# Kernel optimization log

Measured on AMD Instinct MI355X. Metric: run time of the kernel, lower is better.

## Reference

```python
import math
import jax, jax.numpy as jnp
import numpy as np

N, H, E, K = 8192, 2048, 8, 2
CF = 1.25


def setup_inputs() -> dict:
    key = jax.random.key(0)
    ks = jax.random.split(key, 5)
    s1 = 1.0 / math.sqrt(H)
    s2 = 1.0 / math.sqrt(2 * H)
    return {
        "tokens": jax.random.normal(ks[0], (N, H), jnp.float32),
        "Wr": jax.random.normal(ks[1], (E, H), jnp.float32) * s1,   # router: logits = x @ Wr.T + br
        "br": jnp.zeros((E,), jnp.float32),
        "W1": jax.random.normal(ks[2], (E, H, 2 * H), jnp.float32) * s1,
        "b1": jnp.zeros((E, 2 * H), jnp.float32),
        "W2": jax.random.normal(ks[3], (E, 2 * H, H), jnp.float32) * s2,
        "b2": jnp.zeros((E, H), jnp.float32),
    }


def reference(tokens, Wr, br, W1, b1, W2, b2):
    n = tokens.shape[0]
    cap = max(1, math.ceil(CF * n / E))  # per-expert capacity (static)

    # --- router + top-k ---
    logits = tokens @ Wr.T + br                         # [N, E]
    scores, expert_ids = jax.lax.top_k(logits, K)       # [N, K]
    probs = jax.nn.softmax(scores, axis=-1)

    # --- flatten dispatches and sort by expert (stable, like the torch code) ---
    flat_e = expert_ids.reshape(-1)                     # [N*K]
    flat_t = jnp.repeat(jnp.arange(n), K)               # [N*K]
    flat_s = probs.reshape(-1).astype(tokens.dtype)     # [N*K]
    order = jnp.argsort(flat_e)                         # jnp.argsort is stable
    se, st, ss = flat_e[order], flat_t[order], flat_s[order]

    # --- capacity-limited gather: fixed [E, cap] index grid ---
    seg_start = jnp.searchsorted(se, jnp.arange(E))     # [E] first slot of each expert segment
    counts = jnp.bincount(se, length=E)                 # [E] tokens routed to each expert
    slot = jnp.arange(cap)
    idx = jnp.clip(seg_start[:, None] + slot[None, :], 0, n * K - 1)  # [E, cap]
    valid = slot[None, :] < jnp.minimum(counts, cap)[:, None]          # [E, cap]
    tok_idx = st[idx]                                   # [E, cap] source token ids
    w = jnp.where(valid, ss[idx], 0.0)[..., None]       # [E, cap, 1] combine weights (0 => dropped)

    # --- grouped per-expert FFN (GEMM over [E, cap, H]) ---
    x = tokens[tok_idx]                                 # [E, cap, H]
    h = jax.nn.gelu(jnp.einsum('ech,ehf->ecf', x, W1) + b1[:, None, :], approximate=False)
    y = jnp.einsum('ecf,efh->ech', h, W2) + b2[:, None, :]

    # --- weighted scatter-add combine ---
    out = jnp.zeros_like(tokens).at[tok_idx.reshape(-1)].add((y * w).reshape(-1, tokens.shape[-1]))
    return out
```

## Files before the change

### kernel.cpp

```cpp
#include <hip/hip_runtime.h>
#include <hip/hip_bf16.h>
#include <math.h>

#define NTOK 8192
#define HDIM 2048
#define NEXP 8
#define TOPK 2
#define CAP  1280
#define FF   4096

typedef float  f32x4  __attribute__((ext_vector_type(4)));
typedef __bf16 bf16x8 __attribute__((ext_vector_type(8)));

__device__ __forceinline__ ushort f2bf(float f) {
    union { float f; unsigned u; } c; c.f = f;
    unsigned u = c.u;
    unsigned r = (u + 0x7FFFu + ((u >> 16) & 1u)) >> 16;
    return (ushort)r;
}
__device__ __forceinline__ float bf2f(ushort h) {
    union { unsigned u; float f; } c; c.u = ((unsigned)h) << 16;
    return c.f;
}

__global__ void k_convert(const float* __restrict__ src, ushort* __restrict__ dst) {
    int i = (blockIdx.x * 256 + threadIdx.x) * 8;
    float4 a = *(const float4*)(src + i);
    float4 b = *(const float4*)(src + i + 4);
    uint4 o;
    o.x = (unsigned)f2bf(a.x) | ((unsigned)f2bf(a.y) << 16);
    o.y = (unsigned)f2bf(a.z) | ((unsigned)f2bf(a.w) << 16);
    o.z = (unsigned)f2bf(b.x) | ((unsigned)f2bf(b.y) << 16);
    o.w = (unsigned)f2bf(b.z) | ((unsigned)f2bf(b.w) << 16);
    *(uint4*)(dst + i) = o;
}

__global__ void k_router(const float* __restrict__ tokens, const float* __restrict__ Wr,
                         const float* __restrict__ br, int* __restrict__ eids,
                         float* __restrict__ probs) {
    int wave = threadIdx.x >> 6, lane = threadIdx.x & 63;
    int t = blockIdx.x * 4 + wave;
    const float* tp = tokens + (size_t)t * HDIM;
    double acc[NEXP];
    #pragma unroll
    for (int e = 0; e < NEXP; ++e) acc[e] = 0.0;
    for (int j = 0; j < HDIM / 64; ++j) {
        float x = tp[j * 64 + lane];
        #pragma unroll
        for (int e = 0; e < NEXP; ++e)
            acc[e] += (double)x * (double)Wr[e * HDIM + j * 64 + lane];
    }
    #pragma unroll
    for (int e = 0; e < NEXP; ++e) {
        #pragma unroll
        for (int off = 32; off; off >>= 1) acc[e] += __shfl_xor(acc[e], off, 64);
    }
    if (lane == 0) {
        float lg[NEXP];
        #pragma unroll
        for (int e = 0; e < NEXP; ++e) lg[e] = (float)acc[e] + br[e];
        int e0 = 0; float s0 = lg[0];
        #pragma unroll
        for (int e = 1; e < NEXP; ++e) if (lg[e] > s0) { s0 = lg[e]; e0 = e; }
        int e1 = -1; float s1 = -1e30f;
        #pragma unroll
        for (int e = 0; e < NEXP; ++e) if (e != e0 && lg[e] > s1) { s1 = lg[e]; e1 = e; }
        float ex = expf(s1 - s0);
        float den = 1.f + ex;
        eids[t * 2] = e0; eids[t * 2 + 1] = e1;
        probs[t * 2] = 1.f / den; probs[t * 2 + 1] = ex / den;
    }
}

__global__ void k_assign(const int* __restrict__ eids, int* __restrict__ tok_map,
                         int* __restrict__ dest) {
    __shared__ int cnt[64][NEXP];
    int l = threadIdx.x;
    for (int i = l; i < NEXP * CAP; i += 64) tok_map[i] = 0;
    int c[NEXP];
    #pragma unroll
    for (int e = 0; e < NEXP; ++e) c[e] = 0;
    const int base = l * 256;
    for (int i = 0; i < 256; ++i) {
        int ee = eids[base + i];
        #pragma unroll
        for (int e = 0; e < NEXP; ++e) c[e] += (ee == e);
    }
    #pragma unroll
    for (int e = 0; e < NEXP; ++e) cnt[l][e] = c[e];
    __syncthreads();
    if (l < NEXP) {
        int run = 0;
        for (int b = 0; b < 64; ++b) { int v = cnt[b][l]; cnt[b][l] = run; run += v; }
    }
    __syncthreads();
    int off[NEXP];
    #pragma unroll
    for (int e = 0; e < NEXP; ++e) off[e] = cnt[l][e];
    for (int i = 0; i < 256; ++i) {
        int d = base + i;
        int ee = eids[d];
        int r = -1;
        #pragma unroll
        for (int e = 0; e < NEXP; ++e) { bool m = (ee == e); if (m) r = off[e]; off[e] += m; }
        if (r < CAP) { tok_map[ee * CAP + r] = d >> 1; dest[d] = ee * CAP + r; }
        else dest[d] = -1;
    }
}

__global__ void k_transpose(const float* __restrict__ src, ushort* __restrict__ dst,
                            int Kd, int Nd) {
    __shared__ float t[32][33];
    int e = blockIdx.z;
    int k0 = blockIdx.x * 32, n0 = blockIdx.y * 32;
    const float* s = src + (size_t)e * Kd * Nd;
    ushort* d = dst + (size_t)e * Kd * Nd;
    int tid = threadIdx.x;
    #pragma unroll
    for (int i = 0; i < 4; ++i) {
        int idx = i * 256 + tid; int kk = idx >> 5, nn = idx & 31;
        t[kk][nn] = s[(size_t)(k0 + kk) * Nd + n0 + nn];
    }
    __syncthreads();
    #pragma unroll
    for (int i = 0; i < 4; ++i) {
        int idx = i * 256 + tid; int nn = idx >> 5, kk = idx & 31;
        d[(size_t)(n0 + nn) * Kd + k0 + kk] = f2bf(t[kk][nn]);
    }
}

#define LDA 40
template<bool DOGELU, bool GATHER>
__global__ __launch_bounds__(256) void k_gemm(const ushort* __restrict__ A,
                                              const int* __restrict__ tmap,
                                              const ushort* __restrict__ B,
                                              const float* __restrict__ bias,
                                              ushort* __restrict__ C,
                                              int Kd, int Nd) {
    __shared__ ushort As[128 * LDA];
    __shared__ ushort Bs[128 * LDA];
    const int tid = threadIdx.x;
    const int lane = tid & 63;
    const int wave = tid >> 6;
    const int wr = wave >> 1, wc = wave & 1;
    const int e = blockIdx.z;
    const int bm0 = blockIdx.y * 128, bn0 = blockIdx.x * 128;

    const ushort* Be = B + (size_t)e * Nd * Kd;
    const int R  = tid >> 2;
    const int kc = (tid & 3) * 8;
    int ra0, ra1;
    if (GATHER) { ra0 = tmap[e * CAP + bm0 + R]; ra1 = tmap[e * CAP + bm0 + R + 64]; }
    else        { ra0 = e * CAP + bm0 + R;       ra1 = e * CAP + bm0 + R + 64; }
    const ushort* pa0 = A + (size_t)ra0 * Kd + kc;
    const ushort* pa1 = A + (size_t)ra1 * Kd + kc;
    const ushort* pb0 = Be + (size_t)(bn0 + R) * Kd + kc;
    const ushort* pb1 = Be + (size_t)(bn0 + R + 64) * Kd + kc;
    const int sa0 = R * LDA + kc, sa1 = (R + 64) * LDA + kc;

    const int fr = lane & 15, kg = (lane >> 4) * 8;
    f32x4 acc[4][4] = {};

    for (int k0 = 0; k0 < Kd; k0 += 32) {
        uint4 av0 = *(const uint4*)(pa0 + k0);
        uint4 av1 = *(const uint4*)(pa1 + k0);
        uint4 bv0 = *(const uint4*)(pb0 + k0);
        uint4 bv1 = *(const uint4*)(pb1 + k0);
        __syncthreads();
        *(uint4*)(As + sa0) = av0;
        *(uint4*)(As + sa1) = av1;
        *(uint4*)(Bs + sa0) = bv0;
        *(uint4*)(Bs + sa1) = bv1;
        __syncthreads();
        bf16x8 af[4], bfr[4];
        #pragma unroll
        for (int mi = 0; mi < 4; ++mi)
            af[mi] = *(const bf16x8*)(As + (wr * 64 + mi * 16 + fr) * LDA + kg);
        #pragma unroll
        for (int ni = 0; ni < 4; ++ni)
            bfr[ni] = *(const bf16x8*)(Bs + (wc * 64 + ni * 16 + fr) * LDA + kg);
        #pragma unroll
        for (int mi = 0; mi < 4; ++mi)
            #pragma unroll
            for (int ni = 0; ni < 4; ++ni)
                acc[mi][ni] = __builtin_amdgcn_mfma_f32_16x16x32_bf16(af[mi], bfr[ni],
                                                                      acc[mi][ni], 0, 0, 0);
    }

    const float* be = bias + e * Nd;
    ushort* Ce = C + (size_t)e * CAP * Nd;
    const int rl = (lane >> 4) * 4, cl = lane & 15;
    #pragma unroll
    for (int mi = 0; mi < 4; ++mi) {
        #pragma unroll
        for (int ni = 0; ni < 4; ++ni) {
            #pragma unroll
            for (int r = 0; r < 4; ++r) {
                int gr = bm0 + wr * 64 + mi * 16 + rl + r;
                int gc = bn0 + wc * 64 + ni * 16 + cl;
                float v = acc[mi][ni][r] + be[gc];
                if (DOGELU) v = 0.5f * v * (1.f + erff(v * 0.70710678118654752f));
                Ce[(size_t)gr * Nd + gc] = f2bf(v);
            }
        }
    }
}

__global__ void k_combine(const ushort* __restrict__ Y, const int* __restrict__ dest,
                          const float* __restrict__ probs, float* __restrict__ out) {
    int t = blockIdx.x;
    int h0 = threadIdx.x * 8;
    int d0 = dest[t * 2], d1 = dest[t * 2 + 1];
    float p0 = d0 >= 0 ? probs[t * 2] : 0.f;
    float p1 = d1 >= 0 ? probs[t * 2 + 1] : 0.f;
    int r0 = d0 >= 0 ? d0 : 0, r1 = d1 >= 0 ? d1 : 0;
    uint4 a = *(const uint4*)(Y + (size_t)r0 * HDIM + h0);
    uint4 b = *(const uint4*)(Y + (size_t)r1 * HDIM + h0);
    float4 o0, o1;
    o0.x = p0 * bf2f(a.x & 0xffff) + p1 * bf2f(b.x & 0xffff);
    o0.y = p0 * bf2f(a.x >> 16)    + p1 * bf2f(b.x >> 16);
    o0.z = p0 * bf2f(a.y & 0xffff) + p1 * bf2f(b.y & 0xffff);
    o0.w = p0 * bf2f(a.y >> 16)    + p1 * bf2f(b.y >> 16);
    o1.x = p0 * bf2f(a.z & 0xffff) + p1 * bf2f(b.z & 0xffff);
    o1.y = p0 * bf2f(a.z >> 16)    + p1 * bf2f(b.z >> 16);
    o1.z = p0 * bf2f(a.w & 0xffff) + p1 * bf2f(b.w & 0xffff);
    o1.w = p0 * bf2f(a.w >> 16)    + p1 * bf2f(b.w >> 16);
    float* op = out + (size_t)t * HDIM + h0;
    *(float4*)op = o0;
    *(float4*)(op + 4) = o1;
}

extern "C" void kernel_launch(void* const* d_in, const int* in_sizes, int n_in,
                              void* d_out, int out_size, void* d_ws, size_t ws_size,
                              hipStream_t stream) {
    const float* tokens = (const float*)d_in[0];
    const float* Wr     = (const float*)d_in[1];
    const float* br     = (const float*)d_in[2];
    const float* W1     = (const float*)d_in[3];
    const float* b1     = (const float*)d_in[4];
    const float* W2     = (const float*)d_in[5];
    const float* b2     = (const float*)d_in[6];
    float* out = (float*)d_out;
    char* ws = (char*)d_ws;

    int*    eids    = (int*)(ws);
    float*  probs   = (float*)(ws + 65536);
    int*    tok_map = (int*)(ws + 131072);
    int*    dest    = (int*)(ws + 172032);
    size_t off = 1u << 20;
    ushort* TbY = (ushort*)(ws + off);
    off += 41943040;
    ushort* Hm  = (ushort*)(ws + off);
    off += 83886080;
    ushort* WT  = (ushort*)(ws + off);
    (void)in_sizes; (void)n_in; (void)out_size; (void)ws_size;

    k_convert<<<dim3(NTOK * HDIM / 2048), 256, 0, stream>>>(tokens, TbY);
    k_router<<<dim3(NTOK / 4), 256, 0, stream>>>(tokens, Wr, br, eids, probs);
    k_assign<<<dim3(1), 64, 0, stream>>>(eids, tok_map, dest);
    k_transpose<<<dim3(HDIM / 32, FF / 32, NEXP), 256, 0, stream>>>(W1, WT, HDIM, FF);
    k_gemm<true, true><<<dim3(FF / 128, CAP / 128, NEXP), 256, 0, stream>>>(
        TbY, tok_map, WT, b1, Hm, HDIM, FF);
    k_transpose<<<dim3(FF / 32, HDIM / 32, NEXP), 256, 0, stream>>>(W2, WT, FF, HDIM);
    k_gemm<false, false><<<dim3(HDIM / 128, CAP / 128, NEXP), 256, 0, stream>>>(
        Hm, nullptr, WT, b2, TbY, FF, HDIM);
    k_combine<<<dim3(NTOK), 256, 0, stream>>>(TbY, dest, probs, out);
}
```

Measured before the change: 866.0 us.

## Use direct global-to-LDS loads in GEMM and widen weight transpose tiles

The GEMM main loop now loads its A and B tiles with the global_load_lds builtin, so data goes straight from global memory into shared memory instead of passing through registers. The unpadded BK=32 layout matches the per-wave contiguous writes. The weight transpose uses 64x64 tiles with float4 reads and packed 4-element bf16 writes to cut memory transactions. Dropping the LDS padding may bring bank conflicts on the MFMA fragment reads, and the loads are still unpipelined, with a barrier on both sides.

After: 818.7 us. -5.5%, faster.

```diff
diff --git a/kernel.cpp b/kernel.cpp
--- a/kernel.cpp
+++ b/kernel.cpp
@@ -8,9 +8,17 @@
 #define TOPK 2
 #define CAP  1280
 #define FF   4096
+#define BK   32
 
 typedef float  f32x4  __attribute__((ext_vector_type(4)));
 typedef __bf16 bf16x8 __attribute__((ext_vector_type(8)));
+
+typedef __attribute__((address_space(1))) const unsigned int gas_u32;
+typedef __attribute__((address_space(3))) unsigned int las_u32;
+
+__device__ __forceinline__ void gload16(const void* g, void* l) {
+    __builtin_amdgcn_global_load_lds((gas_u32*)g, (las_u32*)l, 16, 0, 0);
+}
 
 __device__ __forceinline__ ushort f2bf(float f) {
     union { float f; unsigned u; } c; c.f = f;
@@ -108,28 +116,34 @@
     }
 }
 
-__global__ void k_transpose(const float* __restrict__ src, ushort* __restrict__ dst,
-                            int Kd, int Nd) {
-    __shared__ float t[32][33];
+__global__ __launch_bounds__(256) void k_transpose(const float* __restrict__ src,
+                                                   ushort* __restrict__ dst,
+                                                   int Kd, int Nd) {
+    __shared__ float tl[64][65];
     int e = blockIdx.z;
-    int k0 = blockIdx.x * 32, n0 = blockIdx.y * 32;
+    int k0 = blockIdx.x * 64, n0 = blockIdx.y * 64;
     const float* s = src + (size_t)e * Kd * Nd;
     ushort* d = dst + (size_t)e * Kd * Nd;
     int tid = threadIdx.x;
     #pragma unroll
     for (int i = 0; i < 4; ++i) {
-        int idx = i * 256 + tid; int kk = idx >> 5, nn = idx & 31;
-        t[kk][nn] = s[(size_t)(k0 + kk) * Nd + n0 + nn];
+        int flat = (i * 256 + tid) * 4;
+        int kk = flat >> 6, nn = flat & 63;
+        float4 v = *(const float4*)(s + (size_t)(k0 + kk) * Nd + n0 + nn);
+        tl[kk][nn] = v.x; tl[kk][nn + 1] = v.y; tl[kk][nn + 2] = v.z; tl[kk][nn + 3] = v.w;
     }
     __syncthreads();
     #pragma unroll
-    for (int i = 0; i < 4; ++i) {
-        int idx = i * 256 + tid; int nn = idx >> 5, kk = idx & 31;
-        d[(size_t)(n0 + nn) * Kd + k0 + kk] = f2bf(t[kk][nn]);
-    }
-}
-
-#define LDA 40
+    for (int g = 0; g < 4; ++g) {
+        int flat = g * 1024 + tid * 4;
+        int nn = flat >> 6, kk = flat & 63;
+        uint2 o;
+        o.x = (unsigned)f2bf(tl[kk][nn])     | ((unsigned)f2bf(tl[kk + 1][nn]) << 16);
+        o.y = (unsigned)f2bf(tl[kk + 2][nn]) | ((unsigned)f2bf(tl[kk + 3][nn]) << 16);
+        *(uint2*)(d + (size_t)(n0 + nn) * Kd + k0 + kk) = o;
+    }
+}
+
 template<bool DOGELU, bool GATHER>
 __global__ __launch_bounds__(256) void k_gemm(const ushort* __restrict__ A,
                                               const int* __restrict__ tmap,
@@ -137,8 +151,8 @@
                                               const float* __restrict__ bias,
                                               ushort* __restrict__ C,
                                               int Kd, int Nd) {
-    __shared__ ushort As[128 * LDA];
-    __shared__ ushort Bs[128 * LDA];
+    __shared__ ushort As[128 * BK];
+    __shared__ ushort Bs[128 * BK];
     const int tid = threadIdx.x;
     const int lane = tid & 63;
     const int wave = tid >> 6;
@@ -156,29 +170,28 @@
     const ushort* pa1 = A + (size_t)ra1 * Kd + kc;
     const ushort* pb0 = Be + (size_t)(bn0 + R) * Kd + kc;
     const ushort* pb1 = Be + (size_t)(bn0 + R + 64) * Kd + kc;
-    const int sa0 = R * LDA + kc, sa1 = (R + 64) * LDA + kc;
+    char* lA0 = (char*)As + wave * 1024;
+    char* lA1 = (char*)As + 4096 + wave * 1024;
+    char* lB0 = (char*)Bs + wave * 1024;
+    char* lB1 = (char*)Bs + 4096 + wave * 1024;
 
     const int fr = lane & 15, kg = (lane >> 4) * 8;
     f32x4 acc[4][4] = {};
 
-    for (int k0 = 0; k0 < Kd; k0 += 32) {
-        uint4 av0 = *(const uint4*)(pa0 + k0);
-        uint4 av1 = *(const uint4*)(pa1 + k0);
-        uint4 bv0 = *(const uint4*)(pb0 + k0);
-        uint4 bv1 = *(const uint4*)(pb1 + k0);
+    for (int k0 = 0; k0 < Kd; k0 += BK) {
         __syncthreads();
-        *(uint4*)(As + sa0) = av0;
-        *(uint4*)(As + sa1) = av1;
-        *(uint4*)(Bs + sa0) = bv0;
-        *(uint4*)(Bs + sa1) = bv1;
+        gload16(pa0 + k0, lA0);
+        gload16(pa1 + k0, lA1);
+        gload16(pb0 + k0, lB0);
+        gload16(pb1 + k0, lB1);
         __syncthreads();
         bf16x8 af[4], bfr[4];
         #pragma unroll
         for (int mi = 0; mi < 4; ++mi)
-            af[mi] = *(const bf16x8*)(As + (wr * 64 + mi * 16 + fr) * LDA + kg);
+            af[mi] = *(const bf16x8*)(As + (wr * 64 + mi * 16 + fr) * BK + kg);
         #pragma unroll
         for (int ni = 0; ni < 4; ++ni)
-            bfr[ni] = *(const bf16x8*)(Bs + (wc * 64 + ni * 16 + fr) * LDA + kg);
+            bfr[ni] = *(const bf16x8*)(Bs + (wc * 64 + ni * 16 + fr) * BK + kg);
         #pragma unroll
         for (int mi = 0; mi < 4; ++mi)
             #pragma unroll
@@ -258,10 +271,10 @@
     k_convert<<<dim3(NTOK * HDIM / 2048), 256, 0, stream>>>(tokens, TbY);
     k_router<<<dim3(NTOK / 4), 256, 0, stream>>>(tokens, Wr, br, eids, probs);
     k_assign<<<dim3(1), 64, 0, stream>>>(eids, tok_map, dest);
-    k_transpose<<<dim3(HDIM / 32, FF / 32, NEXP), 256, 0, stream>>>(W1, WT, HDIM, FF);
+    k_transpose<<<dim3(HDIM / 64, FF / 64, NEXP), 256, 0, stream>>>(W1, WT, HDIM, FF);
     k_gemm<true, true><<<dim3(FF / 128, CAP / 128, NEXP), 256, 0, stream>>>(
         TbY, tok_map, WT, b1, Hm, HDIM, FF);
-    k_transpose<<<dim3(FF / 32, HDIM / 32, NEXP), 256, 0, stream>>>(W2, WT, FF, HDIM);
+    k_transpose<<<dim3(FF / 64, HDIM / 64, NEXP), 256, 0, stream>>>(W2, WT, FF, HDIM);
     k_gemm<false, false><<<dim3(HDIM / 128, CAP / 128, NEXP), 256, 0, stream>>>(
         Hm, nullptr, WT, b2, TbY, FF, HDIM);
     k_combine<<<dim3(NTOK), 256, 0, stream>>>(TbY, dest, probs, out);
```
